# Performance work log

Measured on AMD Instinct MI355X. Metric: run time of the kernel, lower is better.

## Reference

```python
import jax, jax.numpy as jnp
import numpy as np

BS, N, M, D = 4, 8192, 8192, 3

def setup_inputs() -> dict:
    key = jax.random.key(0)
    k1, k2 = jax.random.split(key)
    preds = jax.random.normal(k1, (BS, M, D), dtype=jnp.float32)
    gts = jax.random.normal(k2, (BS, N, D), dtype=jnp.float32)
    mask = jnp.ones((BS, M), dtype=jnp.float32)
    return {"preds": preds, "gts": gts, "mask": mask}

def _pairwise_dist(x, y):
    # x: [bs, N, d] (gts), y: [bs, M, d] (preds)
    # P[b,n,m] = ||x_n||^2 + ||y_m||^2 - 2 x_n . y_m
    rx = jnp.sum(x * x, axis=-1)            # [bs, N] (diag of x @ x^T)
    ry = jnp.sum(y * y, axis=-1)            # [bs, M] (diag of y @ y^T)
    zz = jnp.einsum('bnd,bmd->bnm', x, y)   # [bs, N, M]
    return rx[:, :, None] + ry[:, None, :] - 2.0 * zz

def reference(preds, gts, mask):
    P = _pairwise_dist(gts, preds)          # [bs, N, M]; mask unused (as in source)
    return (jnp.min(P, axis=1),             # [bs, M] min over gts for each pred
            jnp.min(P, axis=2),             # [bs, N] min over preds for each gt
            jnp.argmin(P, axis=1),          # [bs, M]
            jnp.argmin(P, axis=2))          # [bs, N]
```

## Files before the change

kernel.cpp:

```cpp
#include <hip/hip_runtime.h>

#pragma clang fp contract(off)


#define BS     4
#define NPTS   8192
#define CHUNK  1024
#define BLOCK  1024
#define SPLITS 32
#define SLOTS  32
#define QT     8
#define QBLK   (SLOTS * QT)
#define ROWS   (CHUNK / SPLITS)

typedef float f32x2 __attribute__((ext_vector_type(2)));

__global__ __launch_bounds__(BLOCK, 4)
void chamfer_kernel(const float* __restrict__ preds,
                    const float* __restrict__ gts,
                    float* __restrict__ out)
{
#pragma clang fp contract(off)
    const int dir   = blockIdx.z;
    const int b     = blockIdx.y;
    const int t     = threadIdx.x;
    const int slot  = t & (SLOTS - 1);
    const int split = t >> 5;
    const int qb    = blockIdx.x * QBLK;

    const float* qbase = (dir == 0 ? preds : gts) + (size_t)b * NPTS * 3;
    const float* rbase = (dir == 0 ? gts : preds) + (size_t)b * NPTS * 3;
    float* outv = out + (size_t)dir       * BS * NPTS + (size_t)b * NPTS;
    float* outi = out + (size_t)(2 + dir) * BS * NPTS + (size_t)b * NPTS;

    __shared__ float smem[12288];
    float (*sh)[4]        = (float (*)[4])smem;
    float *shv            = smem;
    unsigned short *shi16 = (unsigned short *)(smem + 8192);

    f32x2 qxv[4], qyv[4], qzv[4], rqv[4];
#pragma unroll
    for (int g = 0; g < 4; ++g) {
#pragma unroll
        for (int h = 0; h < 2; ++h) {
            const int j = g * 2 + h;
            const int q = qb + j * SLOTS + slot;
            const float x = qbase[(size_t)q * 3 + 0];
            const float y = qbase[(size_t)q * 3 + 1];
            const float z = qbase[(size_t)q * 3 + 2];
            qxv[g][h] = x; qyv[g][h] = y; qzv[g][h] = z;
            const float a0 = x * x;
            const float a1 = y * y;
            const float a2 = z * z;
            rqv[g][h] = (a0 + a1) + a2;
        }
    }

    float bestv[QT];
    int   besti[QT];
#pragma unroll
    for (int j = 0; j < QT; ++j) { bestv[j] = 3.0e38f; besti[j] = 0; }

    const int nchunks = NPTS / CHUNK;
    for (int c = 0; c < nchunks; ++c) {
        __syncthreads();
        {
            const size_t n = (size_t)c * CHUNK + t;
            const float x = rbase[n * 3 + 0];
            const float y = rbase[n * 3 + 1];
            const float z = rbase[n * 3 + 2];
            sh[t][0] = x;
            sh[t][1] = y;
            sh[t][2] = z;
            const float a0 = x * x;
            const float a1 = y * y;
            const float a2 = z * z;
            sh[t][3] = (a0 + a1) + a2;
        }
        __syncthreads();

        const int row0 = split * ROWS;
#pragma unroll 4
        for (int k = 0; k < ROWS; ++k) {
            const int row = row0 + k;
            const float x  = sh[row][0];
            const float y  = sh[row][1];
            const float z  = sh[row][2];
            const float rr = sh[row][3];
            const int idx = c * CHUNK + row;
#pragma unroll
            for (int g = 0; g < 4; ++g) {
                const f32x2 p0 = qxv[g] * x;
                const f32x2 p1 = qyv[g] * y;
                const f32x2 p2 = qzv[g] * z;
                const f32x2 zz = (p0 + p1) + p2;
                const f32x2 ts = rqv[g] + rr;
                const f32x2 w  = zz * 2.0f;
                const f32x2 v  = ts - w;
                if (v[0] < bestv[2 * g + 0]) { bestv[2 * g + 0] = v[0]; besti[2 * g + 0] = idx; }
                if (v[1] < bestv[2 * g + 1]) { bestv[2 * g + 1] = v[1]; besti[2 * g + 1] = idx; }
            }
        }
    }

    __syncthreads();
#pragma unroll
    for (int j = 0; j < QT; ++j) {
        shv  [split * QBLK + j * SLOTS + slot] = bestv[j];
        shi16[split * QBLK + j * SLOTS + slot] = (unsigned short)besti[j];
    }
    __syncthreads();

    const int qloc = t >> 2;
    const int sl   = t & 3;
    float bv = 3.0e38f;
    int   bi = 0;
#pragma unroll
    for (int k = 0; k < SPLITS / 4; ++k) {
        const int s = sl + k * 4;
        const float v2 = shv[s * QBLK + qloc];
        const int   i2 = shi16[s * QBLK + qloc];
        if (v2 < bv || (v2 == bv && i2 < bi)) { bv = v2; bi = i2; }
    }
#pragma unroll
    for (int o = 1; o < 4; o <<= 1) {
        const float ov = __shfl_xor(bv, o);
        const int   oi = __shfl_xor(bi, o);
        if (ov < bv || (ov == bv && oi < bi)) { bv = ov; bi = oi; }
    }
    if (sl == 0) {
        outv[qb + qloc] = bv;
        outi[qb + qloc] = (float)bi;
    }
}

extern "C" void kernel_launch(void* const* d_in, const int* in_sizes, int n_in,
                              void* d_out, int out_size, void* d_ws, size_t ws_size,
                              hipStream_t stream)
{
    const float* preds = (const float*)d_in[0];
    const float* gts   = (const float*)d_in[1];
    float* out = (float*)d_out;

    dim3 grid(NPTS / QBLK, BS, 2);
    dim3 block(BLOCK);
    chamfer_kernel<<<grid, block, 0, stream>>>(preds, gts, out);
}
```

Before: 117.9 us.

## Pack two reference points per lane with inline v_pk_f32 ops, halve query tile

The kernel now vectorizes across pairs of reference points rather than pairs of query points. It stores x/y and z/r interleaved in LDS so one 16-byte read fetches two reference points, and it forces packed FP32 math through inline v_pk_mul/v_pk_add asm. Queries per thread drop from 8 to 4, which doubles the grid and sets launch bounds to 8 blocks per CU for more occupancy, and the final reduction widens to 8 lanes per query. The cost is less register reuse per LDS read. The hand-written asm may also block compiler scheduling and change rounding behaviour compared with the contract-off scalar code.

```diff
diff --git a/kernel.cpp b/kernel.cpp
--- a/kernel.cpp
+++ b/kernel.cpp
@@ -9,13 +9,31 @@
 #define BLOCK  1024
 #define SPLITS 32
 #define SLOTS  32
-#define QT     8
+#define QT     4
 #define QBLK   (SLOTS * QT)
 #define ROWS   (CHUNK / SPLITS)
+#define RPAIR  (ROWS / 2)
 
 typedef float f32x2 __attribute__((ext_vector_type(2)));
+typedef float f32x4 __attribute__((ext_vector_type(4)));
 
-__global__ __launch_bounds__(BLOCK, 4)
+static __device__ __forceinline__ f32x2 pk_mul(f32x2 a, f32x2 b) {
+    f32x2 d;
+    asm("v_pk_mul_f32 %0, %1, %2" : "=v"(d) : "v"(a), "v"(b));
+    return d;
+}
+static __device__ __forceinline__ f32x2 pk_add(f32x2 a, f32x2 b) {
+    f32x2 d;
+    asm("v_pk_add_f32 %0, %1, %2" : "=v"(d) : "v"(a), "v"(b));
+    return d;
+}
+static __device__ __forceinline__ f32x2 pk_sub(f32x2 a, f32x2 b) {
+    f32x2 d;
+    asm("v_pk_add_f32 %0, %1, %2 neg_lo:[0,1] neg_hi:[0,1]" : "=v"(d) : "v"(a), "v"(b));
+    return d;
+}
+
+__global__ __launch_bounds__(BLOCK, 8)
 void chamfer_kernel(const float* __restrict__ preds,
                     const float* __restrict__ gts,
                     float* __restrict__ out)
@@ -33,33 +51,36 @@
     float* outv = out + (size_t)dir       * BS * NPTS + (size_t)b * NPTS;
     float* outi = out + (size_t)(2 + dir) * BS * NPTS + (size_t)b * NPTS;
 
-    __shared__ float smem[12288];
-    float (*sh)[4]        = (float (*)[4])smem;
-    float *shv            = smem;
-    unsigned short *shi16 = (unsigned short *)(smem + 8192);
+    __shared__ alignas(16) float smem[6144];
+    f32x4* shxy4          = (f32x4*)smem;
+    f32x4* shzr4          = (f32x4*)(smem + 2048);
+    float* shv            = smem;
+    unsigned short* shi16 = (unsigned short*)(smem + 4096);
 
-    f32x2 qxv[4], qyv[4], qzv[4], rqv[4];
+    f32x2 qxx[QT], qyy[QT], qzz[QT], qrr[QT];
 #pragma unroll
-    for (int g = 0; g < 4; ++g) {
-#pragma unroll
-        for (int h = 0; h < 2; ++h) {
-            const int j = g * 2 + h;
-            const int q = qb + j * SLOTS + slot;
-            const float x = qbase[(size_t)q * 3 + 0];
-            const float y = qbase[(size_t)q * 3 + 1];
-            const float z = qbase[(size_t)q * 3 + 2];
-            qxv[g][h] = x; qyv[g][h] = y; qzv[g][h] = z;
-            const float a0 = x * x;
-            const float a1 = y * y;
-            const float a2 = z * z;
-            rqv[g][h] = (a0 + a1) + a2;
-        }
+    for (int j = 0; j < QT; ++j) {
+        const int q = qb + j * SLOTS + slot;
+        const float x = qbase[(size_t)q * 3 + 0];
+        const float y = qbase[(size_t)q * 3 + 1];
+        const float z = qbase[(size_t)q * 3 + 2];
+        const float a0 = x * x;
+        const float a1 = y * y;
+        const float a2 = z * z;
+        const float rq = (a0 + a1) + a2;
+        qxx[j] = (f32x2){x, x};
+        qyy[j] = (f32x2){y, y};
+        qzz[j] = (f32x2){z, z};
+        qrr[j] = (f32x2){rq, rq};
     }
 
     float bestv[QT];
     int   besti[QT];
 #pragma unroll
     for (int j = 0; j < QT; ++j) { bestv[j] = 3.0e38f; besti[j] = 0; }
+
+    float* xy = smem;
+    float* zr = smem + 2048;
 
     const int nchunks = NPTS / CHUNK;
     for (int c = 0; c < nchunks; ++c) {
@@ -69,36 +90,41 @@
             const float x = rbase[n * 3 + 0];
             const float y = rbase[n * 3 + 1];
             const float z = rbase[n * 3 + 2];
-            sh[t][0] = x;
-            sh[t][1] = y;
-            sh[t][2] = z;
             const float a0 = x * x;
             const float a1 = y * y;
             const float a2 = z * z;
-            sh[t][3] = (a0 + a1) + a2;
+            const float rr = (a0 + a1) + a2;
+            const int p  = t >> 1;
+            const int h  = t & 1;
+            xy[p * 4 + h]     = x;
+            xy[p * 4 + 2 + h] = y;
+            zr[p * 4 + h]     = z;
+            zr[p * 4 + 2 + h] = rr;
         }
         __syncthreads();
 
-        const int row0 = split * ROWS;
-#pragma unroll 4
-        for (int k = 0; k < ROWS; ++k) {
-            const int row = row0 + k;
-            const float x  = sh[row][0];
-            const float y  = sh[row][1];
-            const float z  = sh[row][2];
-            const float rr = sh[row][3];
-            const int idx = c * CHUNK + row;
+        const int rp0  = split * RPAIR;
+        const int idxb = c * CHUNK + split * ROWS;
+        for (int k = 0; k < RPAIR; ++k) {
+            const f32x4 axy = shxy4[rp0 + k];
+            const f32x4 azr = shzr4[rp0 + k];
+            const f32x2 xp = (f32x2){axy[0], axy[1]};
+            const f32x2 yp = (f32x2){axy[2], axy[3]};
+            const f32x2 zp = (f32x2){azr[0], azr[1]};
+            const f32x2 rp2 = (f32x2){azr[2], azr[3]};
+            const int idx0 = idxb + 2 * k;
 #pragma unroll
-            for (int g = 0; g < 4; ++g) {
-                const f32x2 p0 = qxv[g] * x;
-                const f32x2 p1 = qyv[g] * y;
-                const f32x2 p2 = qzv[g] * z;
-                const f32x2 zz = (p0 + p1) + p2;
-                const f32x2 ts = rqv[g] + rr;
-                const f32x2 w  = zz * 2.0f;
-                const f32x2 v  = ts - w;
-                if (v[0] < bestv[2 * g + 0]) { bestv[2 * g + 0] = v[0]; besti[2 * g + 0] = idx; }
-                if (v[1] < bestv[2 * g + 1]) { bestv[2 * g + 1] = v[1]; besti[2 * g + 1] = idx; }
+            for (int j = 0; j < QT; ++j) {
+                const f32x2 p0 = pk_mul(xp, qxx[j]);
+                const f32x2 p1 = pk_mul(yp, qyy[j]);
+                const f32x2 s01 = pk_add(p0, p1);
+                const f32x2 p2 = pk_mul(zp, qzz[j]);
+                const f32x2 zz = pk_add(s01, p2);
+                const f32x2 ts = pk_add(rp2, qrr[j]);
+                const f32x2 w  = pk_add(zz, zz);
+                const f32x2 v  = pk_sub(ts, w);
+                if (v[0] < bestv[j]) { bestv[j] = v[0]; besti[j] = idx0; }
+                if (v[1] < bestv[j]) { bestv[j] = v[1]; besti[j] = idx0 + 1; }
             }
         }
     }
@@ -111,19 +137,19 @@
     }
     __syncthreads();
 
-    const int qloc = t >> 2;
-    const int sl   = t & 3;
+    const int qloc = t >> 3;
+    const int sl   = t & 7;
     float bv = 3.0e38f;
     int   bi = 0;
 #pragma unroll
-    for (int k = 0; k < SPLITS / 4; ++k) {
-        const int s = sl + k * 4;
+    for (int k = 0; k < SPLITS / 8; ++k) {
+        const int s = sl + k * 8;
         const float v2 = shv[s * QBLK + qloc];
         const int   i2 = shi16[s * QBLK + qloc];
         if (v2 < bv || (v2 == bv && i2 < bi)) { bv = v2; bi = i2; }
     }
 #pragma unroll
-    for (int o = 1; o < 4; o <<= 1) {
+    for (int o = 1; o < 8; o <<= 1) {
         const float ov = __shfl_xor(bv, o);
         const int   oi = __shfl_xor(bi, o);
         if (ov < bv || (ov == bv && oi < bi)) { bv = ov; bi = oi; }
```

Measured after the change: 118.1 us. No clear change (+0.2%).

## Fuse both chamfer directions into one pass with 64-bit atomicMin column reduction

Applied to the files above, without the earlier changes.

Replaces the two-direction kernel, which computed the full distance matrix twice, with a fused kernel. It computes each distance once and reduces it both along rows, in registers followed by shuffles and shared memory, and along columns, through shuffles and then a packed value/index 64-bit atomicMin into workspace. A memset and a finalize kernel decode the packed keys into values and indices. The old kernel is kept as a fallback when workspace is too small, and its f32x2 packed math is de-vectorised to scalar. The fused path halves the distance arithmetic but adds one global atomic per (block, wavefront, column), plus shuffle reductions and two extra launches.

```diff
diff --git a/kernel.cpp b/kernel.cpp
--- a/kernel.cpp
+++ b/kernel.cpp
@@ -3,22 +3,176 @@
 #pragma clang fp contract(off)
 
 
-#define BS     4
-#define NPTS   8192
+#define BS    4
+#define NPTS  8192
+
+typedef float f32x4 __attribute__((ext_vector_type(4)));
+
+__global__ __launch_bounds__(1024, 4)
+void chamfer_fused(const float* __restrict__ preds,
+                   const float* __restrict__ gts,
+                   float* __restrict__ out,
+                   unsigned long long* __restrict__ colkey)
+{
+#pragma clang fp contract(off)
+    const int b    = blockIdx.y;
+    const int n0   = blockIdx.x * 64;
+    const int t    = threadIdx.x;
+    const int w    = t >> 6;
+    const int lane = t & 63;
+    const int ng   = lane >> 3;
+    const int mg   = lane & 7;
+
+    const float* mb = preds + (size_t)b * NPTS * 3;
+    const float* gb = gts   + (size_t)b * NPTS * 3;
+
+    __shared__ alignas(16) float smem[32768];
+    __shared__ float rs_v[16 * 64];
+    __shared__ int   rs_i[16 * 64];
+    float* xyf = smem;
+    float* zrf = smem + 16384;
+    const f32x4* shxy4 = (const f32x4*)smem;
+    const f32x4* shzr4 = (const f32x4*)(smem + 16384);
+
+    for (int k = 0; k < 8; ++k) {
+        const int p = k * 1024 + t;
+        const float x = mb[p * 3 + 0];
+        const float y = mb[p * 3 + 1];
+        const float z = mb[p * 3 + 2];
+        const float a0 = x * x;
+        const float a1 = y * y;
+        const float a2 = z * z;
+        const float rr = (a0 + a1) + a2;
+        const int pr = p >> 1, h = p & 1;
+        xyf[pr * 4 + h]     = x;
+        xyf[pr * 4 + 2 + h] = y;
+        zrf[pr * 4 + h]     = z;
+        zrf[pr * 4 + 2 + h] = rr;
+    }
+
+    const int nbase = n0 + ng * 8;
+    float qx[8], qy[8], qz[8], rq[8];
+#pragma unroll
+    for (int rn = 0; rn < 8; ++rn) {
+        const int n = nbase + rn;
+        const float x = gb[n * 3 + 0];
+        const float y = gb[n * 3 + 1];
+        const float z = gb[n * 3 + 2];
+        qx[rn] = x; qy[rn] = y; qz[rn] = z;
+        const float a0 = x * x;
+        const float a1 = y * y;
+        const float a2 = z * z;
+        rq[rn] = (a0 + a1) + a2;
+    }
+
+    float rowv[8];
+    int   rowi[8];
+#pragma unroll
+    for (int rn = 0; rn < 8; ++rn) { rowv[rn] = 3.0e38f; rowi[rn] = 0; }
+
+    __syncthreads();
+
+    const int ppbase = w * 256;
+    const unsigned long long* dummy = colkey;  (void)dummy;
+    for (int c = 0; c < 32; ++c) {
+        const int pp = ppbase + c * 8 + mg;
+        const f32x4 axy = shxy4[pp];
+        const f32x4 azr = shzr4[pp];
+        const int m0 = pp * 2;
+#pragma unroll
+        for (int rm = 0; rm < 2; ++rm) {
+            const float mx  = axy[rm];
+            const float my  = axy[2 + rm];
+            const float mz  = azr[rm];
+            const float mrr = azr[2 + rm];
+            const int   mi  = m0 + rm;
+            float cv = 3.0e38f;
+            int   ci = 0;
+#pragma unroll
+            for (int rn = 0; rn < 8; ++rn) {
+                const float p0  = mx * qx[rn];
+                const float p1  = my * qy[rn];
+                const float s01 = p0 + p1;
+                const float p2  = mz * qz[rn];
+                const float zz  = s01 + p2;
+                const float ts = mrr + rq[rn];
+                const float wd = 2.0f * zz;
+                const float v  = ts - wd;
+                if (v < rowv[rn]) { rowv[rn] = v; rowi[rn] = mi; }
+                if (v < cv)       { cv = v;       ci = rn; }
+            }
+            int cn = nbase + ci;
+#pragma unroll
+            for (int o = 8; o < 64; o <<= 1) {
+                const float ov = __shfl_xor(cv, o);
+                const int   on = __shfl_xor(cn, o);
+                if (ov < cv || (ov == cv && on < cn)) { cv = ov; cn = on; }
+            }
+            if (ng == 0) {
+                const unsigned bits = __float_as_uint(cv);
+                const unsigned s = (bits & 0x80000000u) ? ~bits
+                                                        : (bits | 0x80000000u);
+                const unsigned long long key =
+                    ((unsigned long long)s << 32) | (unsigned)cn;
+                atomicMin(&colkey[(size_t)b * NPTS + mi], key);
+            }
+        }
+    }
+
+#pragma unroll
+    for (int rn = 0; rn < 8; ++rn) {
+        float cv = rowv[rn];
+        int   cn = rowi[rn];
+#pragma unroll
+        for (int o = 1; o < 8; o <<= 1) {
+            const float ov = __shfl_xor(cv, o);
+            const int   on = __shfl_xor(cn, o);
+            if (ov < cv || (ov == cv && on < cn)) { cv = ov; cn = on; }
+        }
+        if (mg == 0) {
+            rs_v[w * 64 + ng * 8 + rn] = cv;
+            rs_i[w * 64 + ng * 8 + rn] = cn;
+        }
+    }
+    __syncthreads();
+    if (t < 64) {
+        float bv = rs_v[t];
+        int   bi = rs_i[t];
+        for (int ww = 1; ww < 16; ++ww) {
+            const float v2 = rs_v[ww * 64 + t];
+            const int   i2 = rs_i[ww * 64 + t];
+            if (v2 < bv || (v2 == bv && i2 < bi)) { bv = v2; bi = i2; }
+        }
+        const int n = n0 + t;
+        out[(size_t)(1) * BS * NPTS + (size_t)b * NPTS + n] = bv;
+        out[(size_t)(3) * BS * NPTS + (size_t)b * NPTS + n] = (float)bi;
+    }
+}
+
+__global__ __launch_bounds__(256)
+void chamfer_finalize(const unsigned long long* __restrict__ colkey,
+                      float* __restrict__ out)
+{
+    const int i = blockIdx.x * 256 + threadIdx.x;
+    const unsigned long long k = colkey[i];
+    const unsigned s   = (unsigned)(k >> 32);
+    const unsigned idx = (unsigned)k;
+    const unsigned bits = (s & 0x80000000u) ? (s ^ 0x80000000u) : ~s;
+    out[i] = __uint_as_float(bits);
+    out[(size_t)(2) * BS * NPTS + i] = (float)idx;
+}
+
 #define CHUNK  1024
-#define BLOCK  1024
 #define SPLITS 32
 #define SLOTS  32
 #define QT     8
 #define QBLK   (SLOTS * QT)
 #define ROWS   (CHUNK / SPLITS)
 
-typedef float f32x2 __attribute__((ext_vector_type(2)));
-
-__global__ __launch_bounds__(BLOCK, 4)
-void chamfer_kernel(const float* __restrict__ preds,
-                    const float* __restrict__ gts,
-                    float* __restrict__ out)
+__global__ __launch_bounds__(1024, 4)
+void chamfer_sep(const float* __restrict__ preds,
+                 const float* __restrict__ gts,
+                 float* __restrict__ out)
 {
 #pragma clang fp contract(off)
     const int dir   = blockIdx.z;
@@ -38,67 +192,51 @@
     float *shv            = smem;
     unsigned short *shi16 = (unsigned short *)(smem + 8192);
 
-    f32x2 qxv[4], qyv[4], qzv[4], rqv[4];
-#pragma unroll
-    for (int g = 0; g < 4; ++g) {
-#pragma unroll
-        for (int h = 0; h < 2; ++h) {
-            const int j = g * 2 + h;
-            const int q = qb + j * SLOTS + slot;
-            const float x = qbase[(size_t)q * 3 + 0];
-            const float y = qbase[(size_t)q * 3 + 1];
-            const float z = qbase[(size_t)q * 3 + 2];
-            qxv[g][h] = x; qyv[g][h] = y; qzv[g][h] = z;
-            const float a0 = x * x;
-            const float a1 = y * y;
-            const float a2 = z * z;
-            rqv[g][h] = (a0 + a1) + a2;
-        }
-    }
-
-    float bestv[QT];
-    int   besti[QT];
+    float qxv[QT], qyv[QT], qzv[QT], rqv[QT];
+#pragma unroll
+    for (int j = 0; j < QT; ++j) {
+        const int q = qb + j * SLOTS + slot;
+        const float x = qbase[(size_t)q * 3 + 0];
+        const float y = qbase[(size_t)q * 3 + 1];
+        const float z = qbase[(size_t)q * 3 + 2];
+        qxv[j] = x; qyv[j] = y; qzv[j] = z;
+        const float a0 = x * x, a1 = y * y, a2 = z * z;
+        rqv[j] = (a0 + a1) + a2;
+    }
+
+    float bestv[QT]; int besti[QT];
 #pragma unroll
     for (int j = 0; j < QT; ++j) { bestv[j] = 3.0e38f; besti[j] = 0; }
 
-    const int nchunks = NPTS / CHUNK;
-    for (int c = 0; c < nchunks; ++c) {
+    for (int c = 0; c < NPTS / CHUNK; ++c) {
         __syncthreads();
         {
             const size_t n = (size_t)c * CHUNK + t;
             const float x = rbase[n * 3 + 0];
             const float y = rbase[n * 3 + 1];
             const float z = rbase[n * 3 + 2];
-            sh[t][0] = x;
-            sh[t][1] = y;
-            sh[t][2] = z;
-            const float a0 = x * x;
-            const float a1 = y * y;
-            const float a2 = z * z;
+            sh[t][0] = x; sh[t][1] = y; sh[t][2] = z;
+            const float a0 = x * x, a1 = y * y, a2 = z * z;
             sh[t][3] = (a0 + a1) + a2;
         }
         __syncthreads();
-
         const int row0 = split * ROWS;
 #pragma unroll 4
         for (int k = 0; k < ROWS; ++k) {
             const int row = row0 + k;
-            const float x  = sh[row][0];
-            const float y  = sh[row][1];
-            const float z  = sh[row][2];
-            const float rr = sh[row][3];
+            const float x = sh[row][0], y = sh[row][1];
+            const float z = sh[row][2], rr = sh[row][3];
             const int idx = c * CHUNK + row;
 #pragma unroll
-            for (int g = 0; g < 4; ++g) {
-                const f32x2 p0 = qxv[g] * x;
-                const f32x2 p1 = qyv[g] * y;
-                const f32x2 p2 = qzv[g] * z;
-                const f32x2 zz = (p0 + p1) + p2;
-                const f32x2 ts = rqv[g] + rr;
-                const f32x2 w  = zz * 2.0f;
-                const f32x2 v  = ts - w;
-                if (v[0] < bestv[2 * g + 0]) { bestv[2 * g + 0] = v[0]; besti[2 * g + 0] = idx; }
-                if (v[1] < bestv[2 * g + 1]) { bestv[2 * g + 1] = v[1]; besti[2 * g + 1] = idx; }
+            for (int j = 0; j < QT; ++j) {
+                const float p0 = x * qxv[j];
+                const float p1 = y * qyv[j];
+                const float p2 = z * qzv[j];
+                const float zz = (p0 + p1) + p2;
+                const float ts = rr + rqv[j];
+                const float wd = 2.0f * zz;
+                const float v  = ts - wd;
+                if (v < bestv[j]) { bestv[j] = v; besti[j] = idx; }
             }
         }
     }
@@ -110,11 +248,9 @@
         shi16[split * QBLK + j * SLOTS + slot] = (unsigned short)besti[j];
     }
     __syncthreads();
-
     const int qloc = t >> 2;
     const int sl   = t & 3;
-    float bv = 3.0e38f;
-    int   bi = 0;
+    float bv = 3.0e38f; int bi = 0;
 #pragma unroll
     for (int k = 0; k < SPLITS / 4; ++k) {
         const int s = sl + k * 4;
@@ -128,10 +264,7 @@
         const int   oi = __shfl_xor(bi, o);
         if (ov < bv || (ov == bv && oi < bi)) { bv = ov; bi = oi; }
     }
-    if (sl == 0) {
-        outv[qb + qloc] = bv;
-        outi[qb + qloc] = (float)bi;
-    }
+    if (sl == 0) { outv[qb + qloc] = bv; outi[qb + qloc] = (float)bi; }
 }
 
 extern "C" void kernel_launch(void* const* d_in, const int* in_sizes, int n_in,
@@ -142,7 +275,14 @@
     const float* gts   = (const float*)d_in[1];
     float* out = (float*)d_out;
 
-    dim3 grid(NPTS / QBLK, BS, 2);
-    dim3 block(BLOCK);
-    chamfer_kernel<<<grid, block, 0, stream>>>(preds, gts, out);
-}
+    const size_t need = (size_t)BS * NPTS * sizeof(unsigned long long);
+    if (ws_size >= need) {
+        hipMemsetAsync(d_ws, 0xFF, need, stream);
+        chamfer_fused<<<dim3(NPTS / 64, BS), 1024, 0, stream>>>(
+            preds, gts, out, (unsigned long long*)d_ws);
+        chamfer_finalize<<<dim3(BS * NPTS / 256), 256, 0, stream>>>(
+            (const unsigned long long*)d_ws, out);
+    } else {
+        chamfer_sep<<<dim3(NPTS / QBLK, BS, 2), 1024, 0, stream>>>(preds, gts, out);
+    }
+}
```

After: 154.6 us. 31.1% more time.
